# Kernel tuning notes

Hardware: AMD Instinct MI355X
Metric: run time of the kernel (lower is better)

The kernel has to match this reference:

```python
import jax, jax.numpy as jnp
import numpy as np

N_NODES = 100000
N_EDGES = 1600000
D_IN = 128
D_OUT = 128
LN_EPS = 1e-5
MEAN_EPS = 1e-8


def setup_inputs() -> dict:
    key = jax.random.key(0)
    ks = jax.random.split(key, 8)
    x = jax.random.normal(ks[0], (N_NODES, D_IN), dtype=jnp.float32)
    edge_index = jax.random.randint(ks[1], (2, N_EDGES), 0, N_NODES, dtype=jnp.int64)
    s = 1.0 / np.sqrt(D_IN)
    W_agg = jax.random.uniform(ks[2], (D_OUT, D_IN), jnp.float32, -s, s)
    b_agg = jax.random.uniform(ks[3], (D_OUT,), jnp.float32, -s, s)
    W_self = jax.random.uniform(ks[4], (D_OUT, D_IN), jnp.float32, -s, s)
    b_self = jax.random.uniform(ks[5], (D_OUT,), jnp.float32, -s, s)
    gamma = jnp.ones((D_OUT,), jnp.float32)
    beta = jnp.zeros((D_OUT,), jnp.float32)
    return {"x": x, "edge_index": edge_index, "W_agg": W_agg, "b_agg": b_agg,
            "W_self": W_self, "b_self": b_self, "gamma": gamma, "beta": beta}


def reference(x, edge_index, W_agg, b_agg, W_self, b_self, gamma, beta):
    row, col = edge_index[0], edge_index[1]
    num_nodes = x.shape[0]
    # self path: Linear(in, out)
    self_out = x @ W_self.T + b_self                              # [N, D_OUT]
    # mean aggregation: fused gather + segment-sum (no index_add buffer passes)
    neighbor_sum = jax.ops.segment_sum(x[col], row, num_segments=num_nodes)   # [N, D_IN]
    ones = jnp.ones((col.shape[0], 1), dtype=x.dtype)
    neighbor_count = jax.ops.segment_sum(ones, row, num_segments=num_nodes)   # [N, 1]
    neighbor_mean = neighbor_sum / (neighbor_count + MEAN_EPS)
    agg_out = neighbor_mean @ W_agg.T + b_agg                     # [N, D_OUT]
    # relu -> LayerNorm (dropout is identity at eval)
    h = jax.nn.relu(self_out + agg_out)
    mu = jnp.mean(h, axis=-1, keepdims=True)
    var = jnp.mean(jnp.square(h - mu), axis=-1, keepdims=True)
    return (h - mu) * jax.lax.rsqrt(var + LN_EPS) * gamma + beta
```

## Files before the change

### kernel.cpp

```cpp
#include <hip/hip_runtime.h>

#define N_NODES 100000
#define N_EDGES 1600000
#define D 128
#define RPB 64
#define NBUCKET 1563
#define NBLK 196
#define EPB 8192
#define CHO 1564
#define AGG_CAP 2048
#define XCB 3125
#define SCAN_PAD 1792

constexpr float LN_EPS   = 1e-5f;
constexpr float MEAN_EPS = 1e-8f;

typedef __attribute__((ext_vector_type(8))) short bf16x8;
typedef __attribute__((ext_vector_type(4))) float f32x4;

__device__ inline float bf2f(unsigned short h) {
  union { unsigned u; float f; } v; v.u = (unsigned)h << 16; return v.f;
}
__device__ inline unsigned short f2bf(float f) {
  union { float f; unsigned u; } v; v.f = f;
  return (unsigned short)((v.u + 0x7FFFu + ((v.u >> 16) & 1u)) >> 16);
}

__global__ __launch_bounds__(256) void prep_sort(
    const float* __restrict__ x, const int* __restrict__ ei,
    const float* __restrict__ Wself, const float* __restrict__ Wagg,
    const float* __restrict__ bself, const float* __restrict__ bagg,
    unsigned short* __restrict__ xb, unsigned short* __restrict__ wcat,
    float* __restrict__ bsum, unsigned* __restrict__ ent_sorted,
    int* __restrict__ chunkoff) {
  __shared__ int ent_s[EPB];
  __shared__ int cnt_s[SCAN_PAD];
  __shared__ int off_s[SCAN_PAD];
  __shared__ int sb[256];
  const int bid = blockIdx.x;
  const int t = threadIdx.x;

  if (bid < NBLK) {
    const int ebase = bid * EPB;
    const int nch = min(EPB, N_EDGES - ebase);
    const int base4 = bid * (EPB / 4);
    const int end4 = base4 + (nch >> 2);

    for (int i = t; i < SCAN_PAD; i += 256) cnt_s[i] = 0;
    __syncthreads();

#pragma unroll
    for (int k = 0; k < EPB / 1024; ++k) {
      int i4 = base4 + k * 256 + t;
      if (i4 < end4) {
        int4 r = ((const int4*)ei)[i4];
        atomicAdd(&cnt_s[r.x >> 6], 1);
        atomicAdd(&cnt_s[r.y >> 6], 1);
        atomicAdd(&cnt_s[r.z >> 6], 1);
        atomicAdd(&cnt_s[r.w >> 6], 1);
      }
    }
    __syncthreads();

    int psum = 0;
#pragma unroll
    for (int i = 0; i < 7; ++i) psum += cnt_s[t * 7 + i];
    sb[t] = psum;
    __syncthreads();
    for (int off = 1; off < 256; off <<= 1) {
      int u = (t >= off) ? sb[t - off] : 0;
      __syncthreads();
      sb[t] += u;
      __syncthreads();
    }
    int run = sb[t] - psum;
#pragma unroll
    for (int i = 0; i < 7; ++i) {
      off_s[t * 7 + i] = run;
      run += cnt_s[t * 7 + i];
    }
    __syncthreads();

    for (int b = t; b < NBUCKET; b += 256)
      chunkoff[bid * CHO + b] = off_s[b];
    if (t == 0) chunkoff[bid * CHO + NBUCKET] = nch;
    __syncthreads();

#pragma unroll
    for (int k = 0; k < EPB / 1024; ++k) {
      int i4 = base4 + k * 256 + t;
      if (i4 < end4) {
        int4 r = ((const int4*)ei)[i4];
        int4 c = ((const int4*)(ei + N_EDGES))[i4];
        int p0 = atomicAdd(&off_s[r.x >> 6], 1);
        ent_s[p0] = ((r.x & 63) << 17) | c.x;
        int p1 = atomicAdd(&off_s[r.y >> 6], 1);
        ent_s[p1] = ((r.y & 63) << 17) | c.y;
        int p2 = atomicAdd(&off_s[r.z >> 6], 1);
        ent_s[p2] = ((r.z & 63) << 17) | c.z;
        int p3 = atomicAdd(&off_s[r.w >> 6], 1);
        ent_s[p3] = ((r.w & 63) << 17) | c.w;
      }
    }
    __syncthreads();

    for (int i = t; i < nch; i += 256)
      ent_sorted[ebase + i] = (unsigned)ent_s[i];
  } else if (bid < NBLK + XCB) {
    const int base = (bid - NBLK) * 1024;
#pragma unroll
    for (int k = 0; k < 4; ++k) {
      int i4 = base + k * 256 + t;
      float4 v = ((const float4*)x)[i4];
      ushort4 o;
      o.x = f2bf(v.x); o.y = f2bf(v.y); o.z = f2bf(v.z); o.w = f2bf(v.w);
      ((ushort4*)xb)[i4] = o;
    }
  } else {
    const int blk = bid - NBLK - XCB;
#pragma unroll
    for (int k = 0; k < 8; ++k) {
      int idx = blk * 2048 + k * 256 + t;
      int o = idx >> 8, kc = idx & 255;
      float v = (kc < 128) ? Wself[o * 128 + kc] : Wagg[o * 128 + (kc - 128)];
      wcat[o * 256 + kc] = f2bf(v);
    }
    if (blk == 0 && t < 128) bsum[t] = bself[t] + bagg[t];
  }
}

__global__ __launch_bounds__(256) void aggregate(
    const unsigned short* __restrict__ xb, const unsigned* __restrict__ ent_sorted,
    const int* __restrict__ chunkoff, float* out) {
  __shared__ int ent_s[AGG_CAP];
  __shared__ int col_s[AGG_CAP];
  __shared__ int sb[256];
  __shared__ int cnt_s[RPB];
  __shared__ int off_s[RPB];
  __shared__ int cur_s[RPB];

  const int b = blockIdx.x;
  const int t = threadIdx.x;

  int beg = 0, len = 0;
  if (t < NBLK) {
    beg = chunkoff[t * CHO + b];
    len = chunkoff[t * CHO + b + 1] - beg;
  }
  sb[t] = len;
  __syncthreads();
  for (int off = 1; off < 256; off <<= 1) {
    int u = (t >= off) ? sb[t - off] : 0;
    __syncthreads();
    sb[t] += u;
    __syncthreads();
  }
  int n = sb[255]; if (n > AGG_CAP) n = AGG_CAP;
  int dst = sb[t] - len;
  if (t < NBLK) {
    const unsigned* src = ent_sorted + t * EPB + beg;
    for (int i = 0; i < len; ++i)
      if (dst + i < AGG_CAP) ent_s[dst + i] = (int)src[i];
  }
  __syncthreads();

  if (t < RPB) cnt_s[t] = 0;
  __syncthreads();
  for (int i = t; i < n; i += 256) atomicAdd(&cnt_s[ent_s[i] >> 17], 1);
  __syncthreads();
  if (t < RPB) off_s[t] = cnt_s[t];
  __syncthreads();
  for (int off = 1; off < RPB; off <<= 1) {
    int u = 0;
    if (t < RPB && t >= off) u = off_s[t - off];
    __syncthreads();
    if (t < RPB) off_s[t] += u;
    __syncthreads();
  }
  int excl = 0;
  if (t < RPB) excl = off_s[t] - cnt_s[t];
  __syncthreads();
  if (t < RPB) { off_s[t] = excl; cur_s[t] = excl; }
  __syncthreads();
  for (int i = t; i < n; i += 256) {
    int e = ent_s[i];
    int pos = atomicAdd(&cur_s[e >> 17], 1);
    col_s[pos] = e & 0x1FFFF;
  }
  __syncthreads();

  const int w = t >> 6, lane = t & 63;
  const int grp = lane >> 4, l = lane & 15;
  const int nodebase = b << 6;
  for (int lrow = w; lrow < RPB; lrow += 4) {
    int node = nodebase + lrow;
    if (node >= N_NODES) break;
    int rbeg = off_s[lrow];
    int deg = cnt_s[lrow];
    float acc[8];
#pragma unroll
    for (int k = 0; k < 8; ++k) acc[k] = 0.f;
    for (int j0 = 0; j0 < deg; j0 += 4) {
      int jj = j0 + grp;
      if (jj < deg) {
        int col = col_s[rbeg + jj];
        uint4 p = *(const uint4*)(xb + (size_t)col * D + l * 8);
        acc[0] += bf2f((unsigned short)(p.x & 0xFFFFu));
        acc[1] += bf2f((unsigned short)(p.x >> 16));
        acc[2] += bf2f((unsigned short)(p.y & 0xFFFFu));
        acc[3] += bf2f((unsigned short)(p.y >> 16));
        acc[4] += bf2f((unsigned short)(p.z & 0xFFFFu));
        acc[5] += bf2f((unsigned short)(p.z >> 16));
        acc[6] += bf2f((unsigned short)(p.w & 0xFFFFu));
        acc[7] += bf2f((unsigned short)(p.w >> 16));
      }
    }
#pragma unroll
    for (int k = 0; k < 8; ++k) {
      acc[k] += __shfl_xor(acc[k], 16, 64);
      acc[k] += __shfl_xor(acc[k], 32, 64);
    }
    if (grp == 0) {
      float inv = 1.0f / ((float)deg + MEAN_EPS);
      uint4 o;
      o.x = (unsigned)f2bf(acc[0] * inv) | ((unsigned)f2bf(acc[1] * inv) << 16);
      o.y = (unsigned)f2bf(acc[2] * inv) | ((unsigned)f2bf(acc[3] * inv) << 16);
      o.z = (unsigned)f2bf(acc[4] * inv) | ((unsigned)f2bf(acc[5] * inv) << 16);
      o.w = (unsigned)f2bf(acc[6] * inv) | ((unsigned)f2bf(acc[7] * inv) << 16);
      ((uint4*)(out + (size_t)node * D))[l] = o;
    }
  }
}

__global__ __launch_bounds__(512) void gemm_mfma_ln(
    const unsigned short* __restrict__ xb, const float* out_mean,
    const unsigned short* __restrict__ wcat, const float* __restrict__ bsum,
    const float* __restrict__ gamma, const float* __restrict__ beta,
    float* out) {
  __shared__ unsigned short As[128 * 264];
  __shared__ unsigned short Bs[128 * 264];
  __shared__ float bias_s[128];

  const int t = threadIdx.x;
  const int w = t >> 6, lane = t & 63;
  const int q = lane >> 4, s = lane & 15;
  const int base = blockIdx.x * 128;

  if (t < 128) bias_s[t] = bsum[t];

#pragma unroll
  for (int r = 0; r < 8; ++r) {
    int f = r * 512 + t;
    int row = f >> 5, c = f & 31;
    uint4 v = *(const uint4*)(wcat + row * 256 + c * 8);
    *(uint4*)(Bs + row * 264 + c * 8) = v;
  }
#pragma unroll
  for (int r = 0; r < 8; ++r) {
    int f = r * 512 + t;
    int row = f >> 5, c = f & 31;
    int node = base + row;
    uint4 v = make_uint4(0, 0, 0, 0);
    if (node < N_NODES) {
      const unsigned short* src = (c < 16)
          ? xb + (size_t)node * 128 + c * 8
          : (const unsigned short*)(out_mean + (size_t)node * 128) + (c - 16) * 8;
      v = *(const uint4*)src;
    }
    *(uint4*)(As + row * 264 + c * 8) = v;
  }
  __syncthreads();

  const int mrow = (w & 3) * 32;
  const int ncol = (w >> 2) * 64;

  f32x4 acc[2][4];
#pragma unroll
  for (int i = 0; i < 2; ++i)
#pragma unroll
    for (int j = 0; j < 4; ++j) acc[i][j] = (f32x4)(0.0f);

#pragma unroll
  for (int kk = 0; kk < 8; ++kk) {
    int ko = kk * 32 + q * 8;
    bf16x8 a0 = *(const bf16x8*)(As + (mrow + s) * 264 + ko);
    bf16x8 a1 = *(const bf16x8*)(As + (mrow + 16 + s) * 264 + ko);
    bf16x8 bv[4];
#pragma unroll
    for (int j = 0; j < 4; ++j)
      bv[j] = *(const bf16x8*)(Bs + (ncol + j * 16 + s) * 264 + ko);
#pragma unroll
    for (int j = 0; j < 4; ++j) {
      acc[0][j] = __builtin_amdgcn_mfma_f32_16x16x32_bf16(a0, bv[j], acc[0][j], 0, 0, 0);
      acc[1][j] = __builtin_amdgcn_mfma_f32_16x16x32_bf16(a1, bv[j], acc[1][j], 0, 0, 0);
    }
  }
  __syncthreads();

  float* hS = (float*)As;
#pragma unroll
  for (int i = 0; i < 2; ++i)
#pragma unroll
    for (int j = 0; j < 4; ++j)
#pragma unroll
      for (int r = 0; r < 4; ++r) {
        int row = mrow + i * 16 + q * 4 + r;
        int col = ncol + j * 16 + s;
        float h = acc[i][j][r] + bias_s[col];
        hS[row * 132 + col] = fmaxf(h, 0.0f);
      }
  __syncthreads();

  float gx = gamma[2 * lane], gy = gamma[2 * lane + 1];
  float bx = beta[2 * lane],  by = beta[2 * lane + 1];
#pragma unroll 4
  for (int rr = 0; rr < 16; ++rr) {
    int row = w * 16 + rr;
    int node = base + row;
    float v0 = hS[row * 132 + 2 * lane];
    float v1 = hS[row * 132 + 2 * lane + 1];
    float s1 = v0 + v1, s2 = v0 * v0 + v1 * v1;
#pragma unroll
    for (int m = 1; m < 64; m <<= 1) {
      s1 += __shfl_xor(s1, m, 64);
      s2 += __shfl_xor(s2, m, 64);
    }
    float mu = s1 * (1.0f / 128.0f);
    float var = s2 * (1.0f / 128.0f) - mu * mu;
    float rstd = rsqrtf(var + LN_EPS);
    if (node < N_NODES) {
      float2 o;
      o.x = (v0 - mu) * rstd * gx + bx;
      o.y = (v1 - mu) * rstd * gy + by;
      *(float2*)(out + (size_t)node * 128 + 2 * lane) = o;
    }
  }
}

extern "C" void kernel_launch(void* const* d_in, const int* in_sizes, int n_in,
                              void* d_out, int out_size, void* d_ws, size_t ws_size,
                              hipStream_t stream) {
  const float* x     = (const float*)d_in[0];
  const int*   ei    = (const int*)d_in[1];
  const float* Wagg  = (const float*)d_in[2];
  const float* bagg  = (const float*)d_in[3];
  const float* Wself = (const float*)d_in[4];
  const float* bself = (const float*)d_in[5];
  const float* gamma = (const float*)d_in[6];
  const float* beta  = (const float*)d_in[7];
  float* out = (float*)d_out;

  unsigned short* xb   = (unsigned short*)d_ws;
  unsigned short* wcat = xb + (size_t)N_NODES * D;
  float* bsum      = (float*)(wcat + 128 * 256);
  unsigned* ent_sorted = (unsigned*)(bsum + 128);
  int* chunkoff    = (int*)(ent_sorted + (size_t)NBLK * EPB);

  prep_sort<<<NBLK + XCB + 16, 256, 0, stream>>>(
      x, ei, Wself, Wagg, bself, bagg, xb, wcat, bsum, ent_sorted, chunkoff);

  aggregate<<<NBUCKET, 256, 0, stream>>>(xb, ent_sorted, chunkoff, out);

  gemm_mfma_ln<<<(N_NODES + 127) / 128, 512, 0, stream>>>(
      xb, out, wcat, bsum, gamma, beta, out);
}
```

Before: 238.5 us.

## Restructure aggregation gather, transpose chunk offsets, and register-resident GEMM+LayerNorm

The chunk offset table is now stored transposed and packed as offset|count, so each aggregate block reads one contiguous coalesced row. The neighbour gather gives each lane 2 bf16 features of a row and unrolls 8 neighbours at a time, which replaces the 4-group split with cross-group shuffles. The GEMM now has each wave own 16 rows and all 128 columns, loads A straight from global into registers without an LDS staging tile, and does bias, ReLU and LayerNorm in registers with a 16-lane shuffle reduction. This drops the As buffer and two barriers and raises occupancy via launch_bounds(512,4). In exchange the gather now issues narrow 4-byte loads, and the output stores are strided per lane.

Result: faster. 215.4 us (-9.7%).

```diff
diff --git a/kernel.cpp b/kernel.cpp
--- a/kernel.cpp
+++ b/kernel.cpp
@@ -7,7 +7,6 @@
 #define NBUCKET 1563
 #define NBLK 196
 #define EPB 8192
-#define CHO 1564
 #define AGG_CAP 2048
 #define XCB 3125
 #define SCAN_PAD 1792
@@ -20,6 +19,12 @@
 
 __device__ inline float bf2f(unsigned short h) {
   union { unsigned u; float f; } v; v.u = (unsigned)h << 16; return v.f;
+}
+__device__ inline float bflo(unsigned p) {
+  union { unsigned u; float f; } v; v.u = p << 16; return v.f;
+}
+__device__ inline float bfhi(unsigned p) {
+  union { unsigned u; float f; } v; v.u = p & 0xFFFF0000u; return v.f;
 }
 __device__ inline unsigned short f2bf(float f) {
   union { float f; unsigned u; } v; v.f = f;
@@ -82,8 +87,7 @@
     __syncthreads();
 
     for (int b = t; b < NBUCKET; b += 256)
-      chunkoff[bid * CHO + b] = off_s[b];
-    if (t == 0) chunkoff[bid * CHO + NBUCKET] = nch;
+      chunkoff[b * NBLK + bid] = off_s[b] | (cnt_s[b] << 14);
     __syncthreads();
 
 #pragma unroll
@@ -144,8 +148,9 @@
 
   int beg = 0, len = 0;
   if (t < NBLK) {
-    beg = chunkoff[t * CHO + b];
-    len = chunkoff[t * CHO + b + 1] - beg;
+    int pk = chunkoff[b * NBLK + t];
+    beg = pk & 16383;
+    len = pk >> 14;
   }
   sb[t] = len;
   __syncthreads();
@@ -190,54 +195,51 @@
   __syncthreads();
 
   const int w = t >> 6, lane = t & 63;
-  const int grp = lane >> 4, l = lane & 15;
   const int nodebase = b << 6;
   for (int lrow = w; lrow < RPB; lrow += 4) {
     int node = nodebase + lrow;
     if (node >= N_NODES) break;
     int rbeg = off_s[lrow];
     int deg = cnt_s[lrow];
-    float acc[8];
-#pragma unroll
-    for (int k = 0; k < 8; ++k) acc[k] = 0.f;
-    for (int j0 = 0; j0 < deg; j0 += 4) {
-      int jj = j0 + grp;
-      if (jj < deg) {
-        int col = col_s[rbeg + jj];
-        uint4 p = *(const uint4*)(xb + (size_t)col * D + l * 8);
-        acc[0] += bf2f((unsigned short)(p.x & 0xFFFFu));
-        acc[1] += bf2f((unsigned short)(p.x >> 16));
-        acc[2] += bf2f((unsigned short)(p.y & 0xFFFFu));
-        acc[3] += bf2f((unsigned short)(p.y >> 16));
-        acc[4] += bf2f((unsigned short)(p.z & 0xFFFFu));
-        acc[5] += bf2f((unsigned short)(p.z >> 16));
-        acc[6] += bf2f((unsigned short)(p.w & 0xFFFFu));
-        acc[7] += bf2f((unsigned short)(p.w >> 16));
+    float a0 = 0.f, a1 = 0.f;
+    int j = 0;
+    for (; j + 8 <= deg; j += 8) {
+      unsigned p[8];
+#pragma unroll
+      for (int u = 0; u < 8; ++u) {
+        int col = col_s[rbeg + j + u];
+        p[u] = *(const unsigned*)(xb + (size_t)col * D + lane * 2);
       }
-    }
-#pragma unroll
-    for (int k = 0; k < 8; ++k) {
-      acc[k] += __shfl_xor(acc[k], 16, 64);
-      acc[k] += __shfl_xor(acc[k], 32, 64);
-    }
-    if (grp == 0) {
-      float inv = 1.0f / ((float)deg + MEAN_EPS);
-      uint4 o;
-      o.x = (unsigned)f2bf(acc[0] * inv) | ((unsigned)f2bf(acc[1] * inv) << 16);
-      o.y = (unsigned)f2bf(acc[2] * inv) | ((unsigned)f2bf(acc[3] * inv) << 16);
-      o.z = (unsigned)f2bf(acc[4] * inv) | ((unsigned)f2bf(acc[5] * inv) << 16);
-      o.w = (unsigned)f2bf(acc[6] * inv) | ((unsigned)f2bf(acc[7] * inv) << 16);
-      ((uint4*)(out + (size_t)node * D))[l] = o;
-    }
-  }
-}
-
-__global__ __launch_bounds__(512) void gemm_mfma_ln(
+#pragma unroll
+      for (int u = 0; u < 8; ++u) { a0 += bflo(p[u]); a1 += bfhi(p[u]); }
+    }
+    if (j + 4 <= deg) {
+      unsigned p[4];
+#pragma unroll
+      for (int u = 0; u < 4; ++u) {
+        int col = col_s[rbeg + j + u];
+        p[u] = *(const unsigned*)(xb + (size_t)col * D + lane * 2);
+      }
+#pragma unroll
+      for (int u = 0; u < 4; ++u) { a0 += bflo(p[u]); a1 += bfhi(p[u]); }
+      j += 4;
+    }
+    for (; j < deg; ++j) {
+      int col = col_s[rbeg + j];
+      unsigned p = *(const unsigned*)(xb + (size_t)col * D + lane * 2);
+      a0 += bflo(p); a1 += bfhi(p);
+    }
+    float inv = 1.0f / ((float)deg + MEAN_EPS);
+    unsigned o = (unsigned)f2bf(a0 * inv) | ((unsigned)f2bf(a1 * inv) << 16);
+    ((unsigned*)(out + (size_t)node * D))[lane] = o;
+  }
+}
+
+__global__ __launch_bounds__(512, 4) void gemm_mfma_ln(
     const unsigned short* __restrict__ xb, const float* out_mean,
     const unsigned short* __restrict__ wcat, const float* __restrict__ bsum,
     const float* __restrict__ gamma, const float* __restrict__ beta,
     float* out) {
-  __shared__ unsigned short As[128 * 264];
   __shared__ unsigned short Bs[128 * 264];
   __shared__ float bias_s[128];
 
@@ -255,84 +257,72 @@
     uint4 v = *(const uint4*)(wcat + row * 256 + c * 8);
     *(uint4*)(Bs + row * 264 + c * 8) = v;
   }
-#pragma unroll
-  for (int r = 0; r < 8; ++r) {
-    int f = r * 512 + t;
-    int row = f >> 5, c = f & 31;
-    int node = base + row;
-    uint4 v = make_uint4(0, 0, 0, 0);
-    if (node < N_NODES) {
-      const unsigned short* src = (c < 16)
-          ? xb + (size_t)node * 128 + c * 8
-          : (const unsigned short*)(out_mean + (size_t)node * 128) + (c - 16) * 8;
-      v = *(const uint4*)src;
-    }
-    *(uint4*)(As + row * 264 + c * 8) = v;
-  }
-  __syncthreads();
-
-  const int mrow = (w & 3) * 32;
-  const int ncol = (w >> 2) * 64;
-
-  f32x4 acc[2][4];
-#pragma unroll
-  for (int i = 0; i < 2; ++i)
-#pragma unroll
-    for (int j = 0; j < 4; ++j) acc[i][j] = (f32x4)(0.0f);
+
+  const int arow = base + w * 16 + s;
+  const int asafe = (arow < N_NODES) ? arow : 0;
+  const unsigned short* xrow = xb + (size_t)asafe * 128;
+  const unsigned short* mrow = (const unsigned short*)(out_mean + (size_t)asafe * 128);
+  bf16x8 a[8];
+#pragma unroll
+  for (int kk = 0; kk < 4; ++kk)
+    a[kk] = *(const bf16x8*)(xrow + kk * 32 + q * 8);
+#pragma unroll
+  for (int kk = 0; kk < 4; ++kk)
+    a[4 + kk] = *(const bf16x8*)(mrow + kk * 32 + q * 8);
+
+  __syncthreads();
+
+  f32x4 acc[8];
+#pragma unroll
+  for (int j = 0; j < 8; ++j) acc[j] = (f32x4)(0.0f);
 
 #pragma unroll
   for (int kk = 0; kk < 8; ++kk) {
-    int ko = kk * 32 + q * 8;
-    bf16x8 a0 = *(const bf16x8*)(As + (mrow + s) * 264 + ko);
-    bf16x8 a1 = *(const bf16x8*)(As + (mrow + 16 + s) * 264 + ko);
-    bf16x8 bv[4];
-#pragma unroll
-    for (int j = 0; j < 4; ++j)
-      bv[j] = *(const bf16x8*)(Bs + (ncol + j * 16 + s) * 264 + ko);
-#pragma unroll
-    for (int j = 0; j < 4; ++j) {
-      acc[0][j] = __builtin_amdgcn_mfma_f32_16x16x32_bf16(a0, bv[j], acc[0][j], 0, 0, 0);
-      acc[1][j] = __builtin_amdgcn_mfma_f32_16x16x32_bf16(a1, bv[j], acc[1][j], 0, 0, 0);
-    }
-  }
-  __syncthreads();
-
-  float* hS = (float*)As;
-#pragma unroll
-  for (int i = 0; i < 2; ++i)
-#pragma unroll
-    for (int j = 0; j < 4; ++j)
-#pragma unroll
-      for (int r = 0; r < 4; ++r) {
-        int row = mrow + i * 16 + q * 4 + r;
-        int col = ncol + j * 16 + s;
-        float h = acc[i][j][r] + bias_s[col];
-        hS[row * 132 + col] = fmaxf(h, 0.0f);
-      }
-  __syncthreads();
-
-  float gx = gamma[2 * lane], gy = gamma[2 * lane + 1];
-  float bx = beta[2 * lane],  by = beta[2 * lane + 1];
-#pragma unroll 4
-  for (int rr = 0; rr < 16; ++rr) {
-    int row = w * 16 + rr;
-    int node = base + row;
-    float v0 = hS[row * 132 + 2 * lane];
-    float v1 = hS[row * 132 + 2 * lane + 1];
-    float s1 = v0 + v1, s2 = v0 * v0 + v1 * v1;
-#pragma unroll
-    for (int m = 1; m < 64; m <<= 1) {
+    const int ko = kk * 32 + q * 8;
+#pragma unroll
+    for (int j = 0; j < 8; ++j) {
+      bf16x8 bv = *(const bf16x8*)(Bs + (j * 16 + s) * 264 + ko);
+      acc[j] = __builtin_amdgcn_mfma_f32_16x16x32_bf16(a[kk], bv, acc[j], 0, 0, 0);
+    }
+  }
+
+#pragma unroll
+  for (int j = 0; j < 8; ++j) {
+    float bb = bias_s[j * 16 + s];
+#pragma unroll
+    for (int r = 0; r < 4; ++r)
+      acc[j][r] = fmaxf(acc[j][r] + bb, 0.0f);
+  }
+
+  float g[8], be[8];
+#pragma unroll
+  for (int j = 0; j < 8; ++j) {
+    g[j]  = gamma[j * 16 + s];
+    be[j] = beta[j * 16 + s];
+  }
+
+#pragma unroll
+  for (int r = 0; r < 4; ++r) {
+    float s1 = 0.f, s2 = 0.f;
+#pragma unroll
+    for (int j = 0; j < 8; ++j) {
+      float h = acc[j][r];
+      s1 += h; s2 += h * h;
+    }
+#pragma unroll
+    for (int m = 1; m < 16; m <<= 1) {
       s1 += __shfl_xor(s1, m, 64);
       s2 += __shfl_xor(s2, m, 64);
     }
-    float mu = s1 * (1.0f / 128.0f);
-    float var = s2 * (1.0f / 128.0f) - mu * mu;
-    float rstd = rsqrtf(var + LN_EPS);
+    int node = base + w * 16 + q * 4 + r;
     if (node < N_NODES) {
-      float2 o;
-      o.x = (v0 - mu) * rstd * gx + bx;
-      o.y = (v1 - mu) * rstd * gy + by;
-      *(float2*)(out + (size_t)node * 128 + 2 * lane) = o;
+      float mu = s1 * (1.0f / 128.0f);
+      float var = s2 * (1.0f / 128.0f) - mu * mu;
+      float rstd = rsqrtf(var + LN_EPS);
+      float* orow = out + (size_t)node * 128;
+#pragma unroll
+      for (int j = 0; j < 8; ++j)
+        orow[j * 16 + s] = (acc[j][r] - mu) * rstd * g[j] + be[j];
     }
   }
 }
```
